# Performance work log

Hardware: AMD Instinct MI355X
Metric: run time of the kernel (lower is better)

## Reference

```python
import jax, jax.numpy as jnp
import numpy as np

H = 8            # n_heads
L = 5            # local_context_length


def _local_project(x, pad, W, b):
    """Conv-projected local sliding-window reweighting.
    x: [A,B,S,D], pad: [A,B,L-1,D], W: [D,D] (1x1 conv weight), b: [D].
    Returns [A,B,S,D]."""
    A, B, S, D = x.shape
    xp = jnp.transpose(x, (1, 3, 0, 2))          # [B,D,A,S]
    pp = jnp.transpose(pad, (1, 3, 0, 2))        # [B,D,A,L-1]
    xc = jnp.concatenate([pp, xp], axis=-1)      # [B,D,A,S+L-1]
    xc = jnp.einsum('od,bdas->boas', W, xc) + b[None, :, None, None]
    y = jnp.transpose(xc, (0, 2, 3, 1))          # [B,A,S+L-1,D]
    center = y[:, :, L - 1:, :]                  # [B,A,S,D]
    idx = jnp.arange(S)[:, None] + jnp.arange(L)[None, :]   # [S,L]
    win = y[:, :, idx, :]                        # [B,A,S,L,D]
    scores = jnp.einsum('basd,basld->basl', center, win) / jnp.sqrt(jnp.float32(D))
    w = jax.nn.softmax(scores, axis=-1)          # [B,A,S,L]
    # Faithful to torch: concat windows along dim2 ([B,A,S*L,D]) then
    # view as [B,A,L,S,D] (reinterprets memory, mixing windows) and sum dim 2.
    flat = (w[..., None] * win).reshape(B, A, S * L, D).reshape(B, A, L, S, D)
    out = jnp.sum(flat, axis=2)                  # [B,A,S,D]
    return jnp.transpose(out, (1, 0, 2, 3))      # [A,B,S,D]


def _split_heads(x):
    N, S, D = x.shape
    return jnp.swapaxes(x.reshape(N, S, H, D // H), 1, 2)   # [N,H,S,dk]


def _attention(q, k, v):
    dk = q.shape[-1]
    s = jnp.einsum('nhqd,nhkd->nhqk', q, k) / jnp.sqrt(jnp.float32(dk))
    p = jax.nn.softmax(s, axis=-1)
    return jnp.einsum('nhqk,nhkd->nhqd', p, v)


def setup_inputs() -> dict:
    rng = jax.random.key(0)
    ks = jax.random.split(rng, 12)
    A, B, S, D = 16, 16, 128, 512
    d = {
        'query': jax.random.normal(ks[0], (A, B, S, D), jnp.float32),
        'key': jax.random.normal(ks[1], (A, B, S, D), jnp.float32),
        'value': jax.random.normal(ks[2], (A, B, S, D), jnp.float32),
        'mask': jnp.ones((1, S, S), jnp.int32),
        'padding_price_q': jnp.zeros((A, B, L - 1, D), jnp.float32),
        'padding_price_k': jnp.zeros((A, B, L - 1, D), jnp.float32),
        'Wq': jax.random.normal(ks[3], (D, D), jnp.float32) * 0.02,
        'bq': jnp.zeros((D,), jnp.float32),
        'Wk': jax.random.normal(ks[4], (D, D), jnp.float32) * 0.02,
        'bk': jnp.zeros((D,), jnp.float32),
        'Wv': jax.random.normal(ks[5], (D, D), jnp.float32) * 0.02,
        'bv': jnp.zeros((D,), jnp.float32),
        'Wo': jax.random.normal(ks[6], (D, D), jnp.float32) * 0.02,
        'bo': jnp.zeros((D,), jnp.float32),
    }
    return d


def reference(query, key, value, mask, padding_price_q, padding_price_k,
              Wq, bq, Wk, bk, Wv, bv, Wo, bo):
    A, B, S, D = query.shape
    dk = D // H
    # mask is processed in the original module but never used (attention gets mask=None)
    q = _local_project(query, padding_price_q, Wq, bq).reshape(A * B, S, D)
    k = _local_project(key, padding_price_k, Wk, bk).reshape(A * B, S, D)
    v = jnp.einsum('nsd,od->nso', value.reshape(A * B, S, D), Wv) + bv
    x = _attention(_split_heads(q), _split_heads(k), _split_heads(v))
    x = jnp.swapaxes(x, 1, 2).reshape(A * B, S, D).reshape(A, B, S, D)
    # asset attention (asset_atten=True)
    xa = jnp.transpose(x, (2, 1, 0, 3)).reshape(S * B, A, D)
    h = _split_heads(xa)
    xa = _attention(h, h, h)
    xa = jnp.swapaxes(xa, 1, 2).reshape(S * B, A, D).reshape(S, B, A, D)
    x = jnp.transpose(xa, (2, 1, 0, 3))          # [A,B,S,D]
    return jnp.einsum('absd,od->abso', x, Wo) + bo
```

## Files before the change

### kernel.cpp

```cpp
#include <hip/hip_runtime.h>
#include <math.h>

#define D 512
#define S 128
#define NB 256
#define T132 132

typedef short s16x8 __attribute__((ext_vector_type(8)));
typedef float f32x4 __attribute__((ext_vector_type(4)));
typedef unsigned short ushort;

static inline __device__ float4 ld4(const float* p) { return *(const float4*)p; }
static inline __device__ float4 ld4s(const float* p) { return *(const float4*)p; }
static inline __device__ float2 ld2s(const float* p) { return *(const float2*)p; }

#define GLOAD_LDS16(gp, lp) __builtin_amdgcn_global_load_lds( \
    (const __attribute__((address_space(1))) unsigned int*)(const void*)(gp), \
    (__attribute__((address_space(3))) unsigned int*)(void*)(lp), 16, 0, 0)

static inline __device__ ushort bf16_rtn(float f) {
    unsigned u = __float_as_uint(f);
    unsigned r = u + 0x7FFFu + ((u >> 16) & 1u);
    return (ushort)(r >> 16);
}

__global__ __launch_bounds__(256) void split_rows(
    const float* __restrict__ x, const float* __restrict__ pad,
    ushort* __restrict__ hi, ushort* __restrict__ lo,
    int rowsPerN, int padRows)
{
    int id  = blockIdx.x * 256 + threadIdx.x;
    int row = id >> 6, c8 = (id & 63) * 8;
    int n = row / rowsPerN, r = row - n * rowsPerN;
    const float* src = (r < padRows)
        ? (pad + ((size_t)(n * padRows + r)) * D + c8)
        : (x   + ((size_t)(n * (rowsPerN - padRows) + (r - padRows))) * D + c8);
    float4 f0 = ld4(src), f1 = ld4(src + 4);
    float v[8] = {f0.x,f0.y,f0.z,f0.w,f1.x,f1.y,f1.z,f1.w};
    ushort h[8], l[8];
#pragma unroll
    for (int i = 0; i < 8; ++i) {
        h[i] = bf16_rtn(v[i]);
        float hf = __uint_as_float(((unsigned)h[i]) << 16);
        l[i] = bf16_rtn(v[i] - hf);
    }
    size_t o = (size_t)row * D + c8;
#pragma unroll
    for (int i = 0; i < 4; ++i) {
        ((ushort2*)(hi + o))[i] = make_ushort2(h[2*i], h[2*i+1]);
        ((ushort2*)(lo + o))[i] = make_ushort2(l[2*i], l[2*i+1]);
    }
}

__global__ __launch_bounds__(256, 2) void gemm_mfma_split(
    const ushort* __restrict__ Ahi, const ushort* __restrict__ Alo,
    const ushort* __restrict__ Bhi, const ushort* __restrict__ Blo,
    const float* __restrict__ bias, float* __restrict__ out, int M)
{
    __shared__ ushort lds[32 * 512];
    const int t = threadIdx.x;
    const int wave = t >> 6, lane = t & 63;
    const int wm = wave >> 1, wn = wave & 1;
    const int blockRow = blockIdx.x * 128;
    const int blockCol = blockIdx.y * 128;

    const ushort* gsrc = (wave == 0) ? Ahi : (wave == 1) ? Alo : (wave == 2) ? Bhi : Blo;
    const int rowBase = (wave < 2) ? blockRow : blockCol;
    const int srow = rowBase + (lane & 15);
    const int scol = (lane >> 4) * 8;

    f32x4 acc[4][4];
#pragma unroll
    for (int i = 0; i < 4; ++i)
#pragma unroll
        for (int j = 0; j < 4; ++j) acc[i][j] = (f32x4){0.f,0.f,0.f,0.f};

    for (int k0 = 0; k0 < 512; k0 += 32) {
        __syncthreads();
#pragma unroll
        for (int st = 0; st < 8; ++st) {
            const ushort* gp = gsrc + (size_t)(srow + st * 16) * 512 + k0 + scol;
            GLOAD_LDS16(gp, &lds[(wave * 8 + st) * 512]);
        }
        __syncthreads();

        s16x8 ah[4], al[4], bh[4], bl[4];
#pragma unroll
        for (int i = 0; i < 4; ++i) {
            ah[i] = *(const s16x8*)&lds[( 0 + wm * 4 + i) * 512 + lane * 8];
            al[i] = *(const s16x8*)&lds[( 8 + wm * 4 + i) * 512 + lane * 8];
            bh[i] = *(const s16x8*)&lds[(16 + wn * 4 + i) * 512 + lane * 8];
            bl[i] = *(const s16x8*)&lds[(24 + wn * 4 + i) * 512 + lane * 8];
        }
#pragma unroll
        for (int i = 0; i < 4; ++i)
#pragma unroll
            for (int j = 0; j < 4; ++j) {
                acc[i][j] = __builtin_amdgcn_mfma_f32_16x16x32_bf16(ah[i], bh[j], acc[i][j], 0, 0, 0);
                acc[i][j] = __builtin_amdgcn_mfma_f32_16x16x32_bf16(ah[i], bl[j], acc[i][j], 0, 0, 0);
                acc[i][j] = __builtin_amdgcn_mfma_f32_16x16x32_bf16(al[i], bh[j], acc[i][j], 0, 0, 0);
            }
    }

#pragma unroll
    for (int j = 0; j < 4; ++j) {
        int col = blockCol + (wn * 4 + j) * 16 + (lane & 15);
        float bb = bias[col];
#pragma unroll
        for (int i = 0; i < 4; ++i) {
            int row0 = blockRow + (wm * 4 + i) * 16 + (lane >> 4) * 4;
#pragma unroll
            for (int r = 0; r < 4; ++r)
                out[(size_t)(row0 + r) * 512 + col] = acc[i][j][r] + bb;
        }
    }
}

__global__ __launch_bounds__(256) void win_weights(const float* __restrict__ y,
                                                   float* __restrict__ wbuf)
{
    int g = blockIdx.x * 256 + threadIdx.x;
    int wv = g >> 6, lane = g & 63;
    int n = wv >> 7, s = wv & 127;
    const float* base = y + ((size_t)(n * T132 + s)) * D;
    float4 c0 = ld4(base + 4*D + lane*4);
    float4 c1 = ld4(base + 4*D + 256 + lane*4);
    float sc[5];
#pragma unroll
    for (int j = 0; j < 5; ++j) {
        float4 a0 = ld4(base + j*D + lane*4);
        float4 a1 = ld4(base + j*D + 256 + lane*4);
        float p = c0.x*a0.x + c0.y*a0.y + c0.z*a0.z + c0.w*a0.w
                + c1.x*a1.x + c1.y*a1.y + c1.z*a1.z + c1.w*a1.w;
#pragma unroll
        for (int off = 1; off < 64; off <<= 1) p += __shfl_xor(p, off);
        sc[j] = p * 0.044194173824159216f;
    }
    if (lane == 0) {
        float mx = sc[0];
#pragma unroll
        for (int j = 1; j < 5; ++j) mx = fmaxf(mx, sc[j]);
        float e[5], sum = 0.f;
#pragma unroll
        for (int j = 0; j < 5; ++j) { e[j] = expf(sc[j] - mx); sum += e[j]; }
        float inv = 1.f / sum;
        float* wp = wbuf + ((size_t)(n * 128 + s)) * 5;
#pragma unroll
        for (int j = 0; j < 5; ++j) wp[j] = e[j] * inv;
    }
}

__global__ __launch_bounds__(256) void win_combine(const float* __restrict__ y,
                                                   const float* __restrict__ wbuf,
                                                   float* __restrict__ outq)
{
    int g = blockIdx.x * 256 + threadIdx.x;
    int wv = g >> 6, lane = g & 63;
    int n = wv >> 7, s2 = wv & 127;
    float4 a0 = {0,0,0,0}, a1 = {0,0,0,0};
#pragma unroll
    for (int l2 = 0; l2 < 5; ++l2) {
        int f = l2 * 128 + s2;
        int sidx = f / 5;
        int l = f - sidx * 5;
        float wt = wbuf[((size_t)(n * 128 + sidx)) * 5 + l];
        const float* r = y + ((size_t)(n * T132 + sidx + l)) * D;
        float4 v0 = ld4(r + lane*4), v1 = ld4(r + 256 + lane*4);
        a0.x += wt*v0.x; a0.y += wt*v0.y; a0.z += wt*v0.z; a0.w += wt*v0.w;
        a1.x += wt*v1.x; a1.y += wt*v1.y; a1.z += wt*v1.z; a1.w += wt*v1.w;
    }
    float* op = outq + ((size_t)(n * 128 + s2)) * D;
    *(float4*)(op + lane*4) = a0;
    *(float4*)(op + 256 + lane*4) = a1;
}

__global__ __launch_bounds__(256, 2) void attn1_kernel(const float* __restrict__ q,
                                                       const float* __restrict__ k,
                                                       const float* __restrict__ v,
                                                       float* __restrict__ x1)
{
    __shared__ ushort lds[32768];

    const int n = blockIdx.x >> 3, h = blockIdx.x & 7;
    const int t = threadIdx.x;
    const int wv = t >> 6, lane = t & 63;
    const int lr = lane & 15, lg = lane >> 4;

    const float* qb = q + ((size_t)n * 128) * D + h * 64;
    const float* kb = k + ((size_t)n * 128) * D + h * 64;
    const float* vb = v + ((size_t)n * 128) * D + h * 64;

#pragma unroll
    for (int it = 0; it < 4; ++it) {
        int slot = t + 256 * it;
        int c = slot >> 6, cl = slot & 63;
        int row = (c >> 1) * 16 + (cl & 15);
        int kc  = (c & 1) * 32 + (cl >> 4) * 8;
        const float* src = kb + (size_t)row * D + kc;
        float4 f0 = ld4(src), f1 = ld4(src + 4);
        float vv[8] = {f0.x,f0.y,f0.z,f0.w,f1.x,f1.y,f1.z,f1.w};
        s16x8 hb, lb;
#pragma unroll
        for (int j = 0; j < 8; ++j) {
            ushort hu = bf16_rtn(vv[j]);
            hb[j] = (short)hu;
            lb[j] = (short)bf16_rtn(vv[j] - __uint_as_float(((unsigned)hu) << 16));
        }
        *(s16x8*)&lds[        c * 512 + cl * 8] = hb;
        *(s16x8*)&lds[ 8192 + c * 512 + cl * 8] = lb;
    }
#pragma unroll
    for (int it = 0; it < 4; ++it) {
        int slot = t + 256 * it;
        int c = slot >> 6, cl = slot & 63;
        int d  = (c >> 2) * 16 + (cl & 15);
        int kr = (c & 3) * 32 + (cl >> 4) * 8;
        const float* src = vb + (size_t)kr * D + d;
        s16x8 hb, lb;
#pragma unroll
        for (int j = 0; j < 8; ++j) {
            float f = src[(size_t)j * D];
            ushort hu = bf16_rtn(f);
            hb[j] = (short)hu;
            lb[j] = (short)bf16_rtn(f - __uint_as_float(((unsigned)hu) << 16));
        }
        *(s16x8*)&lds[16384 + c * 512 + cl * 8] = hb;
        *(s16x8*)&lds[24576 + c * 512 + cl * 8] = lb;
    }
    s16x8 qh[2][2], ql[2][2];
#pragma unroll
    for (int mf = 0; mf < 2; ++mf)
#pragma unroll
        for (int ks = 0; ks < 2; ++ks) {
            const float* src = qb + (size_t)(wv*32 + mf*16 + lr) * D + ks*32 + lg*8;
            float4 f0 = ld4(src), f1 = ld4(src + 4);
            float vv[8] = {f0.x,f0.y,f0.z,f0.w,f1.x,f1.y,f1.z,f1.w};
#pragma unroll
            for (int j = 0; j < 8; ++j) {
                ushort hu = bf16_rtn(vv[j]);
                qh[mf][ks][j] = (short)hu;
                ql[mf][ks][j] = (short)bf16_rtn(vv[j] - __uint_as_float(((unsigned)hu) << 16));
            }
        }

    __syncthreads();

    f32x4 acc[2][8];
#pragma unroll
    for (int mf = 0; mf < 2; ++mf)
#pragma unroll
        for (int nf = 0; nf < 8; ++nf) acc[mf][nf] = (f32x4){0.f,0.f,0.f,0.f};

#pragma unroll
    for (int ks = 0; ks < 2; ++ks)
#pragma unroll
        for (int nf = 0; nf < 8; ++nf) {
            s16x8 kh = *(const s16x8*)&lds[       (nf*2 + ks) * 512 + lane * 8];
            s16x8 kl = *(const s16x8*)&lds[8192 + (nf*2 + ks) * 512 + lane * 8];
#pragma unroll
            for (int mf = 0; mf < 2; ++mf) {
                acc[mf][nf] = __builtin_amdgcn_mfma_f32_16x16x32_bf16(qh[mf][ks], kh, acc[mf][nf], 0, 0, 0);
                acc[mf][nf] = __builtin_amdgcn_mfma_f32_16x16x32_bf16(qh[mf][ks], kl, acc[mf][nf], 0, 0, 0);
                acc[mf][nf] = __builtin_amdgcn_mfma_f32_16x16x32_bf16(ql[mf][ks], kh, acc[mf][nf], 0, 0, 0);
            }
        }

    float lsum[2][4];
#pragma unroll
    for (int mf = 0; mf < 2; ++mf)
#pragma unroll
        for (int r = 0; r < 4; ++r) {
            float m = acc[mf][0][r];
#pragma unroll
            for (int nf = 1; nf < 8; ++nf) m = fmaxf(m, acc[mf][nf][r]);
            m *= 0.125f;
#pragma unroll
            for (int off = 1; off < 16; off <<= 1) m = fmaxf(m, __shfl_xor(m, off));
            float s = 0.f;
#pragma unroll
            for (int nf = 0; nf < 8; ++nf) {
                float p = __expf(acc[mf][nf][r] * 0.125f - m);
                acc[mf][nf][r] = p;
                s += p;
            }
#pragma unroll
            for (int off = 1; off < 16; off <<= 1) s += __shfl_xor(s, off);
            lsum[mf][r] = s;
        }

    __syncthreads();

    float* Pw = (float*)(void*)lds + wv * 1056;
    f32x4 x[2][4];
#pragma unroll
    for (int mf = 0; mf < 2; ++mf)
#pragma unroll
        for (int dc = 0; dc < 4; ++dc) x[mf][dc] = (f32x4){0.f,0.f,0.f,0.f};

#pragma unroll
    for (int ks = 0; ks < 4; ++ks) {
#pragma unroll
        for (int mf = 0; mf < 2; ++mf)
#pragma unroll
            for (int nf2 = 0; nf2 < 2; ++nf2)
#pragma unroll
                for (int r = 0; r < 4; ++r)
                    Pw[(mf*16 + lg*4 + r) * 33 + nf2*16 + lr] = acc[mf][2*ks + nf2][r];
        s16x8 ph[2], pl[2];
#pragma unroll
        for (int mf = 0; mf < 2; ++mf)
#pragma unroll
            for (int j = 0; j < 8; ++j) {
                float f = Pw[(mf*16 + lr) * 33 + lg*8 + j];
                ushort hu = bf16_rtn(f);
                ph[mf][j] = (short)hu;
                pl[mf][j] = (short)bf16_rtn(f - __uint_as_float(((unsigned)hu) << 16));
            }
#pragma unroll
        for (int dc = 0; dc < 4; ++dc) {
            s16x8 vh = *(const s16x8*)&lds[16384 + (dc*4 + ks) * 512 + lane * 8];
            s16x8 vl = *(const s16x8*)&lds[24576 + (dc*4 + ks) * 512 + lane * 8];
#pragma unroll
            for (int mf = 0; mf < 2; ++mf) {
                x[mf][dc] = __builtin_amdgcn_mfma_f32_16x16x32_bf16(ph[mf], vh, x[mf][dc], 0, 0, 0);
                x[mf][dc] = __builtin_amdgcn_mfma_f32_16x16x32_bf16(ph[mf], vl, x[mf][dc], 0, 0, 0);
                x[mf][dc] = __builtin_amdgcn_mfma_f32_16x16x32_bf16(pl[mf], vh, x[mf][dc], 0, 0, 0);
            }
        }
    }

#pragma unroll
    for (int mf = 0; mf < 2; ++mf)
#pragma unroll
        for (int r = 0; r < 4; ++r) {
            float inv = 1.f / lsum[mf][r];
            float* op = x1 + ((size_t)(n*128 + wv*32 + mf*16 + lg*4 + r)) * D + h*64;
#pragma unroll
            for (int dc = 0; dc < 4; ++dc)
                op[dc*16 + lr] = x[mf][dc][r] * inv;
        }
}

__global__ __launch_bounds__(256) void attn2_kernel(const float* __restrict__ x1,
                                                    float* __restrict__ x2)
{
    __shared__ float Xs[16][516];
    __shared__ float Sc[8][16][16];
    int m = blockIdx.x;
    int s = m >> 4, b = m & 15;
    int t = threadIdx.x;
#pragma unroll
    for (int i = 0; i < 8; ++i) {
        int f4 = t + 256 * i;
        int a = f4 >> 7, d4 = f4 & 127;
        float4 vv = ld4(x1 + (((size_t)(a * 16 + b)) * 128 + s) * D + d4*4);
        *(float4*)&Xs[a][d4*4] = vv;
    }
    __syncthreads();
    {
        int h = t >> 5;
        int idx = t & 31;
        int r = idx >> 1;
        int jb = (idx & 1) * 8;
        float4 qv[16];
#pragma unroll
        for (int i = 0; i < 16; ++i) qv[i] = ld4(&Xs[r][h*64 + i*4]);
        for (int j = jb; j < jb + 8; ++j) {
            float sacc = 0.f;
#pragma unroll
            for (int i = 0; i < 16; ++i) {
                float4 kv = ld4(&Xs[j][h*64 + i*4]);
                sacc += qv[i].x*kv.x + qv[i].y*kv.y + qv[i].z*kv.z + qv[i].w*kv.w;
            }
            Sc[h][r][j] = sacc * 0.125f;
        }
    }
    __syncthreads();
    if (t < 128) {
        int h = t >> 4, r = t & 15;
        float* row = &Sc[h][r][0];
        float mx = row[0];
#pragma unroll
        for (int j = 1; j < 16; ++j) mx = fmaxf(mx, row[j]);
        float sum = 0.f;
#pragma unroll
        for (int j = 0; j < 16; ++j) { float e = expf(row[j] - mx); row[j] = e; sum += e; }
        float inv = 1.f / sum;
#pragma unroll
        for (int j = 0; j < 16; ++j) row[j] *= inv;
    }
    __syncthreads();
#pragma unroll
    for (int i = 0; i < 8; ++i) {
        int f4 = t + 256 * i;
        int a = f4 >> 7, d4 = f4 & 127;
        int h = d4 >> 4;
        float4 acc = {0,0,0,0};
#pragma unroll
        for (int j = 0; j < 16; ++j) {
            float wj = Sc[h][a][j];
            float4 vv = ld4(&Xs[j][d4*4]);
            acc.x += wj*vv.x; acc.y += wj*vv.y; acc.z += wj*vv.z; acc.w += wj*vv.w;
        }
        *(float4*)(x2 + (((size_t)(a * 16 + b)) * 128 + s) * D + d4*4) = acc;
    }
}

extern "C" void kernel_launch(void* const* d_in, const int* in_sizes, int n_in,
                              void* d_out, int out_size, void* d_ws, size_t ws_size,
                              hipStream_t stream)
{
    const float* query = (const float*)d_in[0];
    const float* key   = (const float*)d_in[1];
    const float* value = (const float*)d_in[2];
    const float* padq  = (const float*)d_in[4];
    const float* padk  = (const float*)d_in[5];
    const float* Wq = (const float*)d_in[6];  const float* bq = (const float*)d_in[7];
    const float* Wk = (const float*)d_in[8];  const float* bk = (const float*)d_in[9];
    const float* Wv = (const float*)d_in[10]; const float* bv = (const float*)d_in[11];
    const float* Wo = (const float*)d_in[12]; const float* bo = (const float*)d_in[13];
    float* out = (float*)d_out;
    float* W   = (float*)d_ws;

    float* Y   = W;
    float* Q   = W + 17301504;
    float* K   = W + 34078720;
    float* WB  = W + 50855936;
    ushort* Whi = (ushort*)(W + 51019776);
    ushort* Wlo = (ushort*)(W + 51150848);
    float* P5  = W + 51281920;
    float* V   = Y;
    float* X1  = V;
    float* X2  = Q;

    ushort* Hq = (ushort*)Q;
    ushort* Lq = (ushort*)K;
    ushort* Hk = (ushort*)K;
    ushort* Lk = (ushort*)P5;
    ushort* Hh = (ushort*)P5;
    ushort* Lh = Hh + (size_t)16384 * 512;

    dim3 blk(256);
    const int Mbr = NB * T132;
    const int Mh  = 16384;

    split_rows<<<Mbr/4, blk, 0, stream>>>(query, padq, Hq, Lq, T132, 4);
    split_rows<<<128,   blk, 0, stream>>>(Wq, nullptr, Whi, Wlo, 512, 0);
    gemm_mfma_split<<<dim3(Mbr/128, 4), blk, 0, stream>>>(Hq, Lq, Whi, Wlo, bq, Y, Mbr);
    win_weights<<<8192, blk, 0, stream>>>(Y, WB);
    win_combine<<<8192, blk, 0, stream>>>(Y, WB, Q);
    split_rows<<<Mbr/4, blk, 0, stream>>>(key, padk, Hk, Lk, T132, 4);
    split_rows<<<128,   blk, 0, stream>>>(Wk, nullptr, Whi, Wlo, 512, 0);
    gemm_mfma_split<<<dim3(Mbr/128, 4), blk, 0, stream>>>(Hk, Lk, Whi, Wlo, bk, Y, Mbr);
    win_weights<<<8192, blk, 0, stream>>>(Y, WB);
    win_combine<<<8192, blk, 0, stream>>>(Y, WB, K);
    split_rows<<<128, blk, 0, stream>>>(Wv, nullptr, Whi, Wlo, 512, 0);
    for (int h = 0; h < 2; ++h) {
        split_rows<<<Mh/4, blk, 0, stream>>>(value + (size_t)h*Mh*512, nullptr, Hh, Lh, 128, 0);
        gemm_mfma_split<<<dim3(Mh/128, 4), blk, 0, stream>>>(Hh, Lh, Whi, Wlo, bv,
                                                             V + (size_t)h*Mh*512, Mh);
    }
    attn1_kernel<<<2048, blk, 0, stream>>>(Q, K, V, X1);
    attn2_kernel<<<2048, blk, 0, stream>>>(X1, X2);
    split_rows<<<128, blk, 0, stream>>>(Wo, nullptr, Whi, Wlo, 512, 0);
    for (int h = 0; h < 2; ++h) {
        split_rows<<<Mh/4, blk, 0, stream>>>(X2 + (size_t)h*Mh*512, nullptr, Hh, Lh, 128, 0);
        gemm_mfma_split<<<dim3(Mh/128, 4), blk, 0, stream>>>(Hh, Lh, Whi, Wlo, bo,
                                                             out + (size_t)h*Mh*512, Mh);
    }
}
```

Measured before the change: 852.2 us.

## Fuse fp32-to-bf16 hi/lo split of activations into the GEMM load path

The GEMM now loads fp32 activation rows (including the padding-row gather) directly into LDS and splits them into bf16 hi/lo fragments in registers, using the packed convert instruction. This removes the separate split_rows passes over the large activation tensors and their write and re-read of hi/lo buffers. The value and output projections also run as single full-size launches instead of two halves. In exchange, each K-step does more per-wave conversion ALU work and loads fp32 A tiles (twice the bytes of bf16) into LDS, with occupancy hinted up to 3 blocks per CU.

```diff
diff --git a/kernel.cpp b/kernel.cpp
--- a/kernel.cpp
+++ b/kernel.cpp
@@ -22,6 +22,27 @@
     unsigned u = __float_as_uint(f);
     unsigned r = u + 0x7FFFu + ((u >> 16) & 1u);
     return (ushort)(r >> 16);
+}
+
+static inline __device__ unsigned pk_bf16(float a, float b) {
+    unsigned r;
+    asm("v_cvt_pk_bf16_f32 %0, %1, %2" : "=v"(r) : "v"(a), "v"(b));
+    return r;
+}
+
+static inline __device__ void split_frag(float4 a0, float4 a1, s16x8& h, s16x8& l) {
+    float f[8] = {a0.x,a0.y,a0.z,a0.w,a1.x,a1.y,a1.z,a1.w};
+    union U { unsigned u[4]; s16x8 v; } hu, lu;
+#pragma unroll
+    for (int p = 0; p < 4; ++p) {
+        unsigned u = pk_bf16(f[2*p], f[2*p+1]);
+        float h0 = __uint_as_float(u << 16);
+        float h1 = __uint_as_float(u & 0xffff0000u);
+        hu.u[p] = u;
+        lu.u[p] = pk_bf16(f[2*p] - h0, f[2*p+1] - h1);
+    }
+    h = hu.v;
+    l = lu.v;
 }
 
 __global__ __launch_bounds__(256) void split_rows(
@@ -52,22 +73,41 @@
     }
 }
 
-__global__ __launch_bounds__(256, 2) void gemm_mfma_split(
-    const ushort* __restrict__ Ahi, const ushort* __restrict__ Alo,
-    const ushort* __restrict__ Bhi, const ushort* __restrict__ Blo,
-    const float* __restrict__ bias, float* __restrict__ out, int M)
-{
-    __shared__ ushort lds[32 * 512];
+__global__ __launch_bounds__(256, 3) void gemm_mfma_fused(
+    const float* __restrict__ A, const float* __restrict__ pad,
+    const ushort* __restrict__ Whi, const ushort* __restrict__ Wlo,
+    const float* __restrict__ bias, float* __restrict__ out,
+    int rowsPerN, int padRows)
+{
+    __shared__ ushort lds[16384];
     const int t = threadIdx.x;
     const int wave = t >> 6, lane = t & 63;
     const int wm = wave >> 1, wn = wave & 1;
     const int blockRow = blockIdx.x * 128;
     const int blockCol = blockIdx.y * 128;
-
-    const ushort* gsrc = (wave == 0) ? Ahi : (wave == 1) ? Alo : (wave == 2) ? Bhi : Blo;
-    const int rowBase = (wave < 2) ? blockRow : blockCol;
-    const int srow = rowBase + (lane & 15);
-    const int scol = (lane >> 4) * 8;
+    const int lr = lane & 15, lg = lane >> 4;
+
+    const float* rowPtr[4] = {nullptr, nullptr, nullptr, nullptr};
+    const ushort* wPtr = nullptr;
+    if (wave < 2) {
+#pragma unroll
+        for (int st = 0; st < 4; ++st) {
+            int row = blockRow + (wave * 4 + st) * 16 + lr;
+            const float* p;
+            if (padRows > 0) {
+                int n = row / rowsPerN, r = row - n * rowsPerN;
+                p = (r < padRows)
+                    ? pad + ((size_t)(n * padRows + r)) * D
+                    : A   + ((size_t)(n * (rowsPerN - padRows) + (r - padRows))) * D;
+            } else {
+                p = A + (size_t)row * D;
+            }
+            rowPtr[st] = p + lg * 8;
+        }
+    } else {
+        const ushort* wsrc = (wave == 2) ? Whi : Wlo;
+        wPtr = wsrc + (size_t)(blockCol + lr) * 512 + lg * 8;
+    }
 
     f32x4 acc[4][4];
 #pragma unroll
@@ -77,38 +117,49 @@
 
     for (int k0 = 0; k0 < 512; k0 += 32) {
         __syncthreads();
-#pragma unroll
-        for (int st = 0; st < 8; ++st) {
-            const ushort* gp = gsrc + (size_t)(srow + st * 16) * 512 + k0 + scol;
-            GLOAD_LDS16(gp, &lds[(wave * 8 + st) * 512]);
+        if (wave < 2) {
+#pragma unroll
+            for (int st = 0; st < 4; ++st) {
+                GLOAD_LDS16(rowPtr[st] + k0,     &lds[((wave*4 + st)*2 + 0) * 512]);
+                GLOAD_LDS16(rowPtr[st] + k0 + 4, &lds[((wave*4 + st)*2 + 1) * 512]);
+            }
+        } else {
+            const int base = 8192 + (wave - 2) * 4096;
+#pragma unroll
+            for (int st = 0; st < 8; ++st)
+                GLOAD_LDS16(wPtr + (size_t)st * 16 * 512 + k0, &lds[base + st * 512]);
         }
         __syncthreads();
 
-        s16x8 ah[4], al[4], bh[4], bl[4];
+        const float* Af = (const float*)lds;
+        s16x8 bh[4], bl[4];
+#pragma unroll
+        for (int j = 0; j < 4; ++j) {
+            bh[j] = *(const s16x8*)&lds[ 8192 + (wn*4 + j) * 512 + lane * 8];
+            bl[j] = *(const s16x8*)&lds[12288 + (wn*4 + j) * 512 + lane * 8];
+        }
 #pragma unroll
         for (int i = 0; i < 4; ++i) {
-            ah[i] = *(const s16x8*)&lds[( 0 + wm * 4 + i) * 512 + lane * 8];
-            al[i] = *(const s16x8*)&lds[( 8 + wm * 4 + i) * 512 + lane * 8];
-            bh[i] = *(const s16x8*)&lds[(16 + wn * 4 + i) * 512 + lane * 8];
-            bl[i] = *(const s16x8*)&lds[(24 + wn * 4 + i) * 512 + lane * 8];
-        }
-#pragma unroll
-        for (int i = 0; i < 4; ++i)
+            float4 a0 = *(const float4*)&Af[((wm*4 + i)*2 + 0) * 256 + lane * 4];
+            float4 a1 = *(const float4*)&Af[((wm*4 + i)*2 + 1) * 256 + lane * 4];
+            s16x8 ah, al;
+            split_frag(a0, a1, ah, al);
 #pragma unroll
             for (int j = 0; j < 4; ++j) {
-                acc[i][j] = __builtin_amdgcn_mfma_f32_16x16x32_bf16(ah[i], bh[j], acc[i][j], 0, 0, 0);
-                acc[i][j] = __builtin_amdgcn_mfma_f32_16x16x32_bf16(ah[i], bl[j], acc[i][j], 0, 0, 0);
-                acc[i][j] = __builtin_amdgcn_mfma_f32_16x16x32_bf16(al[i], bh[j], acc[i][j], 0, 0, 0);
-            }
+                acc[i][j] = __builtin_amdgcn_mfma_f32_16x16x32_bf16(ah, bh[j], acc[i][j], 0, 0, 0);
+                acc[i][j] = __builtin_amdgcn_mfma_f32_16x16x32_bf16(ah, bl[j], acc[i][j], 0, 0, 0);
+                acc[i][j] = __builtin_amdgcn_mfma_f32_16x16x32_bf16(al, bh[j], acc[i][j], 0, 0, 0);
+            }
+        }
     }
 
 #pragma unroll
     for (int j = 0; j < 4; ++j) {
-        int col = blockCol + (wn * 4 + j) * 16 + (lane & 15);
+        int col = blockCol + (wn * 4 + j) * 16 + lr;
         float bb = bias[col];
 #pragma unroll
         for (int i = 0; i < 4; ++i) {
-            int row0 = blockRow + (wm * 4 + i) * 16 + (lane >> 4) * 4;
+            int row0 = blockRow + (wm * 4 + i) * 16 + lg * 4;
 #pragma unroll
             for (int r = 0; r < 4; ++r)
                 out[(size_t)(row0 + r) * 512 + col] = acc[i][j][r] + bb;
@@ -428,44 +479,26 @@
     float* WB  = W + 50855936;
     ushort* Whi = (ushort*)(W + 51019776);
     ushort* Wlo = (ushort*)(W + 51150848);
-    float* P5  = W + 51281920;
     float* V   = Y;
     float* X1  = V;
     float* X2  = Q;
 
-    ushort* Hq = (ushort*)Q;
-    ushort* Lq = (ushort*)K;
-    ushort* Hk = (ushort*)K;
-    ushort* Lk = (ushort*)P5;
-    ushort* Hh = (ushort*)P5;
-    ushort* Lh = Hh + (size_t)16384 * 512;
-
     dim3 blk(256);
     const int Mbr = NB * T132;
-    const int Mh  = 16384;
-
-    split_rows<<<Mbr/4, blk, 0, stream>>>(query, padq, Hq, Lq, T132, 4);
-    split_rows<<<128,   blk, 0, stream>>>(Wq, nullptr, Whi, Wlo, 512, 0);
-    gemm_mfma_split<<<dim3(Mbr/128, 4), blk, 0, stream>>>(Hq, Lq, Whi, Wlo, bq, Y, Mbr);
+    const int Mfull = 32768;
+
+    split_rows<<<128, blk, 0, stream>>>(Wq, nullptr, Whi, Wlo, 512, 0);
+    gemm_mfma_fused<<<dim3(Mbr/128, 4), blk, 0, stream>>>(query, padq, Whi, Wlo, bq, Y, T132, 4);
     win_weights<<<8192, blk, 0, stream>>>(Y, WB);
     win_combine<<<8192, blk, 0, stream>>>(Y, WB, Q);
-    split_rows<<<Mbr/4, blk, 0, stream>>>(key, padk, Hk, Lk, T132, 4);
-    split_rows<<<128,   blk, 0, stream>>>(Wk, nullptr, Whi, Wlo, 512, 0);
-    gemm_mfma_split<<<dim3(Mbr/128, 4), blk, 0, stream>>>(Hk, Lk, Whi, Wlo, bk, Y, Mbr);
+    split_rows<<<128, blk, 0, stream>>>(Wk, nullptr, Whi, Wlo, 512, 0);
+    gemm_mfma_fused<<<dim3(Mbr/128, 4), blk, 0, stream>>>(key, padk, Whi, Wlo, bk, Y, T132, 4);
     win_weights<<<8192, blk, 0, stream>>>(Y, WB);
     win_combine<<<8192, blk, 0, stream>>>(Y, WB, K);
     split_rows<<<128, blk, 0, stream>>>(Wv, nullptr, Whi, Wlo, 512, 0);
-    for (int h = 0; h < 2; ++h) {
-        split_rows<<<Mh/4, blk, 0, stream>>>(value + (size_t)h*Mh*512, nullptr, Hh, Lh, 128, 0);
-        gemm_mfma_split<<<dim3(Mh/128, 4), blk, 0, stream>>>(Hh, Lh, Whi, Wlo, bv,
-                                                             V + (size_t)h*Mh*512, Mh);
-    }
+    gemm_mfma_fused<<<dim3(Mfull/128, 4), blk, 0, stream>>>(value, nullptr, Whi, Wlo, bv, V, 128, 0);
     attn1_kernel<<<2048, blk, 0, stream>>>(Q, K, V, X1);
     attn2_kernel<<<2048, blk, 0, stream>>>(X1, X2);
     split_rows<<<128, blk, 0, stream>>>(Wo, nullptr, Whi, Wlo, 512, 0);
-    for (int h = 0; h < 2; ++h) {
-        split_rows<<<Mh/4, blk, 0, stream>>>(X2 + (size_t)h*Mh*512, nullptr, Hh, Lh, 128, 0);
-        gemm_mfma_split<<<dim3(Mh/128, 4), blk, 0, stream>>>(Hh, Lh, Whi, Wlo, bo,
-                                                             out + (size_t)h*Mh*512, Mh);
-    }
-}
+    gemm_mfma_fused<<<dim3(Mfull/128, 4), blk, 0, stream>>>(X2, nullptr, Whi, Wlo, bo, out, 128, 0);
+}
```

After: 769.5 us. 9.7% less time.
